# Optimization experiments

Measured on AMD Instinct MI355X. Metric: run time of the kernel, lower is better.

The kernel has to match this reference:

```python
import jax, jax.numpy as jnp
import numpy as np

B, S, D = 2, 2048, 512
H = 8
HD = D // H  # head dim = 64


def setup_inputs() -> dict:
    key = jax.random.key(0)
    ks = jax.random.split(key, 4)
    scale = 1.0 / np.sqrt(D)
    x = jax.random.normal(ks[0], (B, S, D), dtype=jnp.float32)
    wq = jax.random.normal(ks[1], (D, D), dtype=jnp.float32) * scale
    wk = jax.random.normal(ks[2], (D, D), dtype=jnp.float32) * scale
    wv = jax.random.normal(ks[3], (D, D), dtype=jnp.float32) * scale
    bq = jnp.zeros((D,), dtype=jnp.float32)
    bk = jnp.zeros((D,), dtype=jnp.float32)
    bv = jnp.zeros((D,), dtype=jnp.float32)
    return {"x": x, "wq": wq, "bq": bq, "wk": wk, "bk": bk, "wv": wv, "bv": bv}


def reference(x, wq, bq, wk, bk, wv, bv):
    # Linear projections (torch Linear: y = x @ W^T + b; weights here stored as [out,in])
    q = x @ wq.T + bq  # [B,S,D]
    k = x @ wk.T + bk
    v = x @ wv.T + bv
    # split heads -> [B,H,S,HD]
    q = q.reshape(B, S, H, HD).transpose(0, 2, 1, 3)
    k = k.reshape(B, S, H, HD).transpose(0, 2, 1, 3)
    v = v.reshape(B, S, H, HD).transpose(0, 2, 1, 3)
    # QK^T scores, scaled by 1/sqrt(head_dim)
    scores = jnp.einsum("bhqd,bhkd->bhqk", q, k) / jnp.sqrt(jnp.float32(HD))
    # softmax-free: elementwise sigmoid instead of softmax normalization
    attn = jax.nn.sigmoid(scores)  # [B,H,S,S] — the memory-bound intermediate
    out = jnp.einsum("bhqk,bhkd->bhqd", attn, v)
    # merge heads -> [B,S,D]
    return out.transpose(0, 2, 1, 3).reshape(B, S, D)
```

## Files before the change

kernel.cpp:

```cpp
#include <hip/hip_runtime.h>
#include <cstdint>
#include <cstddef>

#define BB   2
#define SS   2048
#define DD   512
#define HH   8
#define HDIM 64

typedef __attribute__((ext_vector_type(8)))  short          s16x8;
typedef __attribute__((ext_vector_type(8)))  unsigned short u16x8;
typedef __attribute__((ext_vector_type(16))) float          f32x16;

static __device__ __forceinline__ unsigned short f2bf(float f) {
  union { float f; unsigned u; } x; x.f = f;
  unsigned r = x.u + 0x7fffu + ((x.u >> 16) & 1u);
  return (unsigned short)(r >> 16);
}
static __device__ __forceinline__ unsigned packtrunc(float lo, float hi) {
  return __builtin_amdgcn_perm(__float_as_uint(hi), __float_as_uint(lo), 0x07060302u);
}

#define QSCALE (-0.18033688011111543f)

__global__ __launch_bounds__(256) void proj_kernel(
    const float* __restrict__ x,
    const float* __restrict__ wq, const float* __restrict__ wk, const float* __restrict__ wv,
    const float* __restrict__ bq, const float* __restrict__ bk, const float* __restrict__ bv,
    unsigned short* __restrict__ qo, unsigned short* __restrict__ ko,
    unsigned short* __restrict__ vt) {
  __shared__ unsigned short As[2][128 * 40];
  __shared__ unsigned short Bs[2][64 * 40];

  const int z = blockIdx.z;
  const float* w; const float* bias;
  if (z == 0)      { w = wq; bias = bq; }
  else if (z == 1) { w = wk; bias = bk; }
  else             { w = wv; bias = bv; }

  const int t = threadIdx.x;
  const int lane = t & 63, wave = t >> 6;
  const int ln = lane & 31, hi = lane >> 5;
  const int m0 = blockIdx.x * 128, n0 = blockIdx.y * 64;

  float4 ar[4], br[2];
#pragma unroll
  for (int i = 0; i < 4; i++) {
    int c = t + i * 256;
    ar[i] = *(const float4*)&x[(size_t)(m0 + (c >> 3)) * DD + (c & 7) * 4];
  }
#pragma unroll
  for (int i = 0; i < 2; i++) {
    int c = t + i * 256;
    br[i] = *(const float4*)&w[(size_t)(n0 + (c >> 3)) * DD + (c & 7) * 4];
  }
#pragma unroll
  for (int i = 0; i < 4; i++) {
    int c = t + i * 256;
    uint2 u; u.x = packtrunc(ar[i].x, ar[i].y); u.y = packtrunc(ar[i].z, ar[i].w);
    *(uint2*)&As[0][(c >> 3) * 40 + (c & 7) * 4] = u;
  }
#pragma unroll
  for (int i = 0; i < 2; i++) {
    int c = t + i * 256;
    uint2 u; u.x = packtrunc(br[i].x, br[i].y); u.y = packtrunc(br[i].z, br[i].w);
    *(uint2*)&Bs[0][(c >> 3) * 40 + (c & 7) * 4] = u;
  }
  __syncthreads();

  f32x16 acc0 = {}, acc1 = {};

#pragma unroll 2
  for (int kt = 0; kt < 16; kt++) {
    const int cur = kt & 1, nxt = cur ^ 1;
    if (kt < 15) {
      int k0 = (kt + 1) * 32;
#pragma unroll
      for (int i = 0; i < 4; i++) {
        int c = t + i * 256;
        ar[i] = *(const float4*)&x[(size_t)(m0 + (c >> 3)) * DD + k0 + (c & 7) * 4];
      }
#pragma unroll
      for (int i = 0; i < 2; i++) {
        int c = t + i * 256;
        br[i] = *(const float4*)&w[(size_t)(n0 + (c >> 3)) * DD + k0 + (c & 7) * 4];
      }
    }
#pragma unroll
    for (int c = 0; c < 2; c++) {
      s16x8 af = *(const s16x8*)&As[cur][(wave * 32 + ln) * 40 + c * 16 + hi * 8];
      s16x8 b0 = *(const s16x8*)&Bs[cur][(ln) * 40 + c * 16 + hi * 8];
      s16x8 b1 = *(const s16x8*)&Bs[cur][(32 + ln) * 40 + c * 16 + hi * 8];
      acc0 = __builtin_amdgcn_mfma_f32_32x32x16_bf16(af, b0, acc0, 0, 0, 0);
      acc1 = __builtin_amdgcn_mfma_f32_32x32x16_bf16(af, b1, acc1, 0, 0, 0);
    }
    if (kt < 15) {
#pragma unroll
      for (int i = 0; i < 4; i++) {
        int c = t + i * 256;
        uint2 u; u.x = packtrunc(ar[i].x, ar[i].y); u.y = packtrunc(ar[i].z, ar[i].w);
        *(uint2*)&As[nxt][(c >> 3) * 40 + (c & 7) * 4] = u;
      }
#pragma unroll
      for (int i = 0; i < 2; i++) {
        int c = t + i * 256;
        uint2 u; u.x = packtrunc(br[i].x, br[i].y); u.y = packtrunc(br[i].z, br[i].w);
        *(uint2*)&Bs[nxt][(c >> 3) * 40 + (c & 7) * 4] = u;
      }
    }
    __syncthreads();
  }

  const float scale = (z == 0) ? QSCALE : 1.0f;
  const int h = blockIdx.y;
  const int bidx = m0 >> 11;
  const int sbase = (m0 & 2047) + wave * 32;
  unsigned short* dst = (z == 0) ? qo : ko;
#pragma unroll
  for (int nh = 0; nh < 2; nh++) {
    f32x16 a = nh ? acc1 : acc0;
    float bval = bias[n0 + nh * 32 + ln];
    int hd = nh * 32 + ln;
    if (z < 2) {
#pragma unroll
      for (int r = 0; r < 16; r++) {
        int s = sbase + (r & 3) + 8 * (r >> 2) + 4 * hi;
        dst[(((size_t)(bidx * HH + h) * SS) + s) * HDIM + hd] = f2bf((a[r] + bval) * scale);
      }
    } else {
      size_t rowbase = (((size_t)(bidx * HH + h) * HDIM) + hd) * SS;
#pragma unroll
      for (int g = 0; g < 4; g++) {
#pragma unroll
        for (int j = 0; j < 4; j += 2) {
          int s = sbase + 8 * g + 4 * hi + j;
          unsigned pk = (unsigned)f2bf(a[g * 4 + j] + bval) |
                        ((unsigned)f2bf(a[g * 4 + j + 1] + bval) << 16);
          *(unsigned*)&vt[rowbase + s] = pk;
        }
      }
    }
  }
}

__global__ __launch_bounds__(256, 2) void attn_kernel(
    const unsigned short* __restrict__ qb,
    const unsigned short* __restrict__ kb,
    const unsigned short* __restrict__ vtb,
    float* __restrict__ out) {
  __shared__ __align__(16) float red[4 * 4096];

  const int t = threadIdx.x;
  const int lane = t & 63, wave = t >> 6;
  const int ln = lane & 31, hi = lane >> 5;
  const int fid = blockIdx.y * 32 + blockIdx.x;
  const int bh = fid & 15, qx = fid >> 4;
  const int b = bh >> 3, h = bh & 7;
  const unsigned short* qp = qb + (size_t)bh * SS * HDIM;
  const unsigned short* kp = kb + (size_t)bh * SS * HDIM;
  const unsigned short* vp = vtb + (size_t)bh * HDIM * SS;
  const int q0 = qx * 64;

  s16x8 qf[2][4];
#pragma unroll
  for (int qs = 0; qs < 2; qs++)
#pragma unroll
    for (int c = 0; c < 4; c++)
      qf[qs][c] = *(const s16x8*)&qp[(size_t)(q0 + qs * 32 + ln) * HDIM + c * 16 + hi * 8];

  f32x16 o00 = {}, o01 = {}, o10 = {}, o11 = {};

  s16x8 kf[2][4], vf[2][4];
  int koff = (wave * 32 + ln) * HDIM + hi * 8;
  int voff = ln * SS + wave * 32 + hi * 8;
#pragma unroll
  for (int c = 0; c < 4; c++) kf[0][c] = *(const s16x8*)&kp[koff + c * 16];
#pragma unroll
  for (int c = 0; c < 2; c++) {
    vf[0][c]     = *(const s16x8*)&vp[voff + c * 16];
    vf[0][2 + c] = *(const s16x8*)&vp[voff + 32 * SS + c * 16];
  }
  koff += 4 * 32 * HDIM;
  voff += 128;

#pragma unroll 2
  for (int i = 0; i < 16; i++) {
    const int cur = i & 1, nxt = cur ^ 1;
    if (i < 15) {
#pragma unroll
      for (int c = 0; c < 4; c++) kf[nxt][c] = *(const s16x8*)&kp[koff + c * 16];
#pragma unroll
      for (int c = 0; c < 2; c++) {
        vf[nxt][c]     = *(const s16x8*)&vp[voff + c * 16];
        vf[nxt][2 + c] = *(const s16x8*)&vp[voff + 32 * SS + c * 16];
      }
      koff += 4 * 32 * HDIM;
      voff += 128;
    }

    f32x16 st0 = {}, st1 = {};
#pragma unroll
    for (int c = 0; c < 4; c++) {
      st0 = __builtin_amdgcn_mfma_f32_32x32x16_bf16(kf[cur][c], qf[0][c], st0, 0, 0, 0);
      st1 = __builtin_amdgcn_mfma_f32_32x32x16_bf16(kf[cur][c], qf[1][c], st1, 0, 0, 0);
    }

    unsigned pgx[2][4], pgy[2][4];
#pragma unroll
    for (int qs = 0; qs < 2; qs++) {
      f32x16 stq = qs ? st1 : st0;
#pragma unroll
      for (int g = 0; g < 4; g++) {
        float p0 = __builtin_amdgcn_rcpf(1.0f + __builtin_amdgcn_exp2f(stq[4 * g + 0]));
        float p1 = __builtin_amdgcn_rcpf(1.0f + __builtin_amdgcn_exp2f(stq[4 * g + 1]));
        float p2 = __builtin_amdgcn_rcpf(1.0f + __builtin_amdgcn_exp2f(stq[4 * g + 2]));
        float p3 = __builtin_amdgcn_rcpf(1.0f + __builtin_amdgcn_exp2f(stq[4 * g + 3]));
        pgx[qs][g] = packtrunc(p0, p1);
        pgy[qs][g] = packtrunc(p2, p3);
      }
    }

#pragma unroll
    for (int c = 0; c < 2; c++) {
      const int gk = 2 * c + hi, gs = 2 * c + (hi ^ 1);
#pragma unroll
      for (int qs = 0; qs < 2; qs++) {
        unsigned rx = __shfl_xor((int)pgx[qs][gs], 32, 64);
        unsigned ry = __shfl_xor((int)pgy[qs][gs], 32, 64);
        union { unsigned u[4]; s16x8 v; } pu;
        pu.u[0] = hi ? rx : pgx[qs][gk];
        pu.u[1] = hi ? ry : pgy[qs][gk];
        pu.u[2] = hi ? pgx[qs][gk] : rx;
        pu.u[3] = hi ? pgy[qs][gk] : ry;
        if (qs == 0) {
          o00 = __builtin_amdgcn_mfma_f32_32x32x16_bf16(pu.v, vf[cur][c], o00, 0, 0, 0);
          o01 = __builtin_amdgcn_mfma_f32_32x32x16_bf16(pu.v, vf[cur][2 + c], o01, 0, 0, 0);
        } else {
          o10 = __builtin_amdgcn_mfma_f32_32x32x16_bf16(pu.v, vf[cur][c], o10, 0, 0, 0);
          o11 = __builtin_amdgcn_mfma_f32_32x32x16_bf16(pu.v, vf[cur][2 + c], o11, 0, 0, 0);
        }
      }
    }
  }

#pragma unroll
  for (int qs = 0; qs < 2; qs++)
#pragma unroll
    for (int dh = 0; dh < 2; dh++) {
      f32x16 ov = qs ? (dh ? o11 : o10) : (dh ? o01 : o00);
#pragma unroll
      for (int r = 0; r < 16; r++) {
        int ql = qs * 32 + (r & 3) + 8 * (r >> 2) + 4 * hi;
        red[wave * 4096 + ql * 64 + dh * 32 + ln] = ov[r];
      }
    }
  __syncthreads();
  const float4* red4 = (const float4*)red;
#pragma unroll
  for (int j = 0; j < 4; j++) {
    int g = t + j * 256;
    float4 s0 = red4[g], s1 = red4[1024 + g], s2 = red4[2048 + g], s3 = red4[3072 + g];
    float4 s;
    s.x = s0.x + s1.x + s2.x + s3.x;
    s.y = s0.y + s1.y + s2.y + s3.y;
    s.z = s0.z + s1.z + s2.z + s3.z;
    s.w = s0.w + s1.w + s2.w + s3.w;
    int q = g >> 4, dbase = (g & 15) * 4;
    *(float4*)&out[((size_t)(b * SS + q0 + q)) * DD + h * HDIM + dbase] = s;
  }
}

extern "C" void kernel_launch(void* const* d_in, const int* in_sizes, int n_in,
                              void* d_out, int out_size, void* d_ws, size_t ws_size,
                              hipStream_t stream) {
  const float* x  = (const float*)d_in[0];
  const float* wq = (const float*)d_in[1];
  const float* bq = (const float*)d_in[2];
  const float* wk = (const float*)d_in[3];
  const float* bk = (const float*)d_in[4];
  const float* wv = (const float*)d_in[5];
  const float* bv = (const float*)d_in[6];
  float* out = (float*)d_out;

  constexpr size_t XN = (size_t)BB * SS * DD;

  unsigned short* qo = (unsigned short*)d_ws;
  unsigned short* ko = qo + XN;
  unsigned short* vt = ko + XN;

  proj_kernel<<<dim3(32, 8, 3), 256, 0, stream>>>(x, wq, wk, wv, bq, bk, bv, qo, ko, vt);
  attn_kernel<<<dim3(SS / 64, BB * HH), 256, 0, stream>>>(qo, ko, vt, out);
}
```

Measured before the change: 125.3 us.

## Pre-swizzle K/V into fragment-contiguous layout and shrink projection tiles

The projection kernel now writes K and V directly in the per-lane MFMA fragment order, so the attention kernel loads each K/V fragment as one contiguous 16-byte chunk per lane instead of strided rows. The projection tile drops from 128x64 to 64x64 with a 2x2 wave grid, doubling its grid size. In the attention kernel the cross-wave reduction buffer is halved by having two waves accumulate in place, and launch bounds are raised to allow 4 blocks per CU. The trade-off is a more complex scattered store pattern in the projection epilogue and an extra synchronisation in the reduction.

New measurement: 334.7 us. 167% more time.

```diff
diff --git a/kernel.cpp b/kernel.cpp
--- a/kernel.cpp
+++ b/kernel.cpp
@@ -29,7 +29,7 @@
     const float* __restrict__ bq, const float* __restrict__ bk, const float* __restrict__ bv,
     unsigned short* __restrict__ qo, unsigned short* __restrict__ ko,
     unsigned short* __restrict__ vt) {
-  __shared__ unsigned short As[2][128 * 40];
+  __shared__ unsigned short As[2][64 * 40];
   __shared__ unsigned short Bs[2][64 * 40];
 
   const int z = blockIdx.z;
@@ -41,34 +41,28 @@
   const int t = threadIdx.x;
   const int lane = t & 63, wave = t >> 6;
   const int ln = lane & 31, hi = lane >> 5;
-  const int m0 = blockIdx.x * 128, n0 = blockIdx.y * 64;
-
-  float4 ar[4], br[2];
-#pragma unroll
-  for (int i = 0; i < 4; i++) {
+  const int wr = wave >> 1, wc = wave & 1;
+  const int m0 = blockIdx.x * 64, n0 = blockIdx.y * 64;
+
+  float4 ar[2], br[2];
+#pragma unroll
+  for (int i = 0; i < 2; i++) {
     int c = t + i * 256;
     ar[i] = *(const float4*)&x[(size_t)(m0 + (c >> 3)) * DD + (c & 7) * 4];
+    br[i] = *(const float4*)&w[(size_t)(n0 + (c >> 3)) * DD + (c & 7) * 4];
   }
 #pragma unroll
   for (int i = 0; i < 2; i++) {
     int c = t + i * 256;
-    br[i] = *(const float4*)&w[(size_t)(n0 + (c >> 3)) * DD + (c & 7) * 4];
-  }
-#pragma unroll
-  for (int i = 0; i < 4; i++) {
-    int c = t + i * 256;
-    uint2 u; u.x = packtrunc(ar[i].x, ar[i].y); u.y = packtrunc(ar[i].z, ar[i].w);
-    *(uint2*)&As[0][(c >> 3) * 40 + (c & 7) * 4] = u;
-  }
-#pragma unroll
-  for (int i = 0; i < 2; i++) {
-    int c = t + i * 256;
-    uint2 u; u.x = packtrunc(br[i].x, br[i].y); u.y = packtrunc(br[i].z, br[i].w);
-    *(uint2*)&Bs[0][(c >> 3) * 40 + (c & 7) * 4] = u;
+    uint2 ua, ub;
+    ua.x = packtrunc(ar[i].x, ar[i].y); ua.y = packtrunc(ar[i].z, ar[i].w);
+    ub.x = packtrunc(br[i].x, br[i].y); ub.y = packtrunc(br[i].z, br[i].w);
+    *(uint2*)&As[0][(c >> 3) * 40 + (c & 7) * 4] = ua;
+    *(uint2*)&Bs[0][(c >> 3) * 40 + (c & 7) * 4] = ub;
   }
   __syncthreads();
 
-  f32x16 acc0 = {}, acc1 = {};
+  f32x16 acc = {};
 
 #pragma unroll 2
   for (int kt = 0; kt < 16; kt++) {
@@ -76,79 +70,76 @@
     if (kt < 15) {
       int k0 = (kt + 1) * 32;
 #pragma unroll
-      for (int i = 0; i < 4; i++) {
+      for (int i = 0; i < 2; i++) {
         int c = t + i * 256;
         ar[i] = *(const float4*)&x[(size_t)(m0 + (c >> 3)) * DD + k0 + (c & 7) * 4];
-      }
+        br[i] = *(const float4*)&w[(size_t)(n0 + (c >> 3)) * DD + k0 + (c & 7) * 4];
+      }
+    }
+#pragma unroll
+    for (int c = 0; c < 2; c++) {
+      s16x8 af = *(const s16x8*)&As[cur][(wr * 32 + ln) * 40 + c * 16 + hi * 8];
+      s16x8 bf = *(const s16x8*)&Bs[cur][(wc * 32 + ln) * 40 + c * 16 + hi * 8];
+      acc = __builtin_amdgcn_mfma_f32_32x32x16_bf16(af, bf, acc, 0, 0, 0);
+    }
+    if (kt < 15) {
 #pragma unroll
       for (int i = 0; i < 2; i++) {
         int c = t + i * 256;
-        br[i] = *(const float4*)&w[(size_t)(n0 + (c >> 3)) * DD + k0 + (c & 7) * 4];
-      }
-    }
-#pragma unroll
-    for (int c = 0; c < 2; c++) {
-      s16x8 af = *(const s16x8*)&As[cur][(wave * 32 + ln) * 40 + c * 16 + hi * 8];
-      s16x8 b0 = *(const s16x8*)&Bs[cur][(ln) * 40 + c * 16 + hi * 8];
-      s16x8 b1 = *(const s16x8*)&Bs[cur][(32 + ln) * 40 + c * 16 + hi * 8];
-      acc0 = __builtin_amdgcn_mfma_f32_32x32x16_bf16(af, b0, acc0, 0, 0, 0);
-      acc1 = __builtin_amdgcn_mfma_f32_32x32x16_bf16(af, b1, acc1, 0, 0, 0);
-    }
-    if (kt < 15) {
-#pragma unroll
-      for (int i = 0; i < 4; i++) {
-        int c = t + i * 256;
-        uint2 u; u.x = packtrunc(ar[i].x, ar[i].y); u.y = packtrunc(ar[i].z, ar[i].w);
-        *(uint2*)&As[nxt][(c >> 3) * 40 + (c & 7) * 4] = u;
-      }
-#pragma unroll
-      for (int i = 0; i < 2; i++) {
-        int c = t + i * 256;
-        uint2 u; u.x = packtrunc(br[i].x, br[i].y); u.y = packtrunc(br[i].z, br[i].w);
-        *(uint2*)&Bs[nxt][(c >> 3) * 40 + (c & 7) * 4] = u;
+        uint2 ua, ub;
+        ua.x = packtrunc(ar[i].x, ar[i].y); ua.y = packtrunc(ar[i].z, ar[i].w);
+        ub.x = packtrunc(br[i].x, br[i].y); ub.y = packtrunc(br[i].z, br[i].w);
+        *(uint2*)&As[nxt][(c >> 3) * 40 + (c & 7) * 4] = ua;
+        *(uint2*)&Bs[nxt][(c >> 3) * 40 + (c & 7) * 4] = ub;
       }
     }
     __syncthreads();
   }
 
-  const float scale = (z == 0) ? QSCALE : 1.0f;
   const int h = blockIdx.y;
   const int bidx = m0 >> 11;
-  const int sbase = (m0 & 2047) + wave * 32;
-  unsigned short* dst = (z == 0) ? qo : ko;
-#pragma unroll
-  for (int nh = 0; nh < 2; nh++) {
-    f32x16 a = nh ? acc1 : acc0;
-    float bval = bias[n0 + nh * 32 + ln];
-    int hd = nh * 32 + ln;
-    if (z < 2) {
-#pragma unroll
-      for (int r = 0; r < 16; r++) {
-        int s = sbase + (r & 3) + 8 * (r >> 2) + 4 * hi;
-        dst[(((size_t)(bidx * HH + h) * SS) + s) * HDIM + hd] = f2bf((a[r] + bval) * scale);
-      }
-    } else {
-      size_t rowbase = (((size_t)(bidx * HH + h) * HDIM) + hd) * SS;
-#pragma unroll
-      for (int g = 0; g < 4; g++) {
-#pragma unroll
-        for (int j = 0; j < 4; j += 2) {
-          int s = sbase + 8 * g + 4 * hi + j;
-          unsigned pk = (unsigned)f2bf(a[g * 4 + j] + bval) |
-                        ((unsigned)f2bf(a[g * 4 + j + 1] + bval) << 16);
-          *(unsigned*)&vt[rowbase + s] = pk;
-        }
-      }
-    }
-  }
-}
-
-__global__ __launch_bounds__(256, 2) void attn_kernel(
+  const int sbase = (m0 & 2047) + wr * 32;
+  const int hd = wc * 32 + ln;
+  const float bval = bias[n0 + hd];
+  const size_t bhb = (size_t)(bidx * HH + h) * SS * HDIM;
+
+  if (z == 0) {
+#pragma unroll
+    for (int r = 0; r < 16; r++) {
+      int s = sbase + (r & 3) + 8 * (r >> 2) + 4 * hi;
+      qo[bhb + (size_t)s * HDIM + hd] = f2bf((acc[r] + bval) * QSCALE);
+    }
+  } else if (z == 1) {
+    const int c = hd >> 4, hk = (hd >> 3) & 1, j = hd & 7;
+    const int kts = sbase >> 5;
+    unsigned short* kd = ko + bhb + ((size_t)kts * 4 + c) * 512 + j;
+#pragma unroll
+    for (int r = 0; r < 16; r++) {
+      int off = (r & 3) + 8 * (r >> 2) + 4 * hi;
+      kd[(hk * 32 + off) * 8] = f2bf(acc[r] + bval);
+    }
+  } else {
+    const int kts = sbase >> 5;
+    unsigned short* vd = vt + bhb + ((size_t)kts * 4 + wc * 2) * 512 + ln * 8 + 4 * hi;
+#pragma unroll
+    for (int g = 0; g < 4; g++) {
+      unsigned short* vg = vd + ((g >> 1) * 512) + (g & 1) * 256;
+#pragma unroll
+      for (int j = 0; j < 4; j += 2) {
+        unsigned pk = (unsigned)f2bf(acc[g * 4 + j] + bval) |
+                      ((unsigned)f2bf(acc[g * 4 + j + 1] + bval) << 16);
+        *(unsigned*)&vg[j] = pk;
+      }
+    }
+  }
+}
+
+__global__ __launch_bounds__(256, 4) void attn_kernel(
     const unsigned short* __restrict__ qb,
-    const unsigned short* __restrict__ kb,
-    const unsigned short* __restrict__ vtb,
+    const unsigned short* __restrict__ kfb,
+    const unsigned short* __restrict__ vfb,
     float* __restrict__ out) {
-  __shared__ __align__(16) float red[4 * 4096];
+  __shared__ __align__(16) float red[2 * 4096];
 
   const int t = threadIdx.x;
   const int lane = t & 63, wave = t >> 6;
@@ -157,8 +148,8 @@
   const int bh = fid & 15, qx = fid >> 4;
   const int b = bh >> 3, h = bh & 7;
   const unsigned short* qp = qb + (size_t)bh * SS * HDIM;
-  const unsigned short* kp = kb + (size_t)bh * SS * HDIM;
-  const unsigned short* vp = vtb + (size_t)bh * HDIM * SS;
+  const unsigned short* kfp = kfb + (size_t)bh * SS * HDIM;
+  const unsigned short* vfp = vfb + (size_t)bh * SS * HDIM;
   const int q0 = qx * 64;
 
   s16x8 qf[2][4];
@@ -171,31 +162,25 @@
   f32x16 o00 = {}, o01 = {}, o10 = {}, o11 = {};
 
   s16x8 kf[2][4], vf[2][4];
-  int koff = (wave * 32 + ln) * HDIM + hi * 8;
-  int voff = ln * SS + wave * 32 + hi * 8;
-#pragma unroll
-  for (int c = 0; c < 4; c++) kf[0][c] = *(const s16x8*)&kp[koff + c * 16];
-#pragma unroll
-  for (int c = 0; c < 2; c++) {
-    vf[0][c]     = *(const s16x8*)&vp[voff + c * 16];
-    vf[0][2 + c] = *(const s16x8*)&vp[voff + 32 * SS + c * 16];
-  }
-  koff += 4 * 32 * HDIM;
-  voff += 128;
+  int koff = wave * 4 * 512 + lane * 8;
+  int voff = koff;
+#pragma unroll
+  for (int c = 0; c < 4; c++) {
+    kf[0][c] = *(const s16x8*)&kfp[koff + c * 512];
+    vf[0][c] = *(const s16x8*)&vfp[voff + c * 512];
+  }
+  koff += 8192; voff += 8192;
 
 #pragma unroll 2
   for (int i = 0; i < 16; i++) {
     const int cur = i & 1, nxt = cur ^ 1;
     if (i < 15) {
 #pragma unroll
-      for (int c = 0; c < 4; c++) kf[nxt][c] = *(const s16x8*)&kp[koff + c * 16];
-#pragma unroll
-      for (int c = 0; c < 2; c++) {
-        vf[nxt][c]     = *(const s16x8*)&vp[voff + c * 16];
-        vf[nxt][2 + c] = *(const s16x8*)&vp[voff + 32 * SS + c * 16];
-      }
-      koff += 4 * 32 * HDIM;
-      voff += 128;
+      for (int c = 0; c < 4; c++) {
+        kf[nxt][c] = *(const s16x8*)&kfp[koff + c * 512];
+        vf[nxt][c] = *(const s16x8*)&vfp[voff + c * 512];
+      }
+      koff += 8192; voff += 8192;
     }
 
     f32x16 st0 = {}, st1 = {};
@@ -243,28 +228,43 @@
     }
   }
 
-#pragma unroll
-  for (int qs = 0; qs < 2; qs++)
-#pragma unroll
-    for (int dh = 0; dh < 2; dh++) {
-      f32x16 ov = qs ? (dh ? o11 : o10) : (dh ? o01 : o00);
-#pragma unroll
-      for (int r = 0; r < 16; r++) {
-        int ql = qs * 32 + (r & 3) + 8 * (r >> 2) + 4 * hi;
-        red[wave * 4096 + ql * 64 + dh * 32 + ln] = ov[r];
-      }
-    }
+  if (wave >= 2) {
+#pragma unroll
+    for (int qs = 0; qs < 2; qs++)
+#pragma unroll
+      for (int dh = 0; dh < 2; dh++) {
+        f32x16 ov = qs ? (dh ? o11 : o10) : (dh ? o01 : o00);
+#pragma unroll
+        for (int r = 0; r < 16; r++) {
+          int ql = qs * 32 + (r & 3) + 8 * (r >> 2) + 4 * hi;
+          red[(wave - 2) * 4096 + ql * 64 + dh * 32 + ln] = ov[r];
+        }
+      }
+  }
   __syncthreads();
-  const float4* red4 = (const float4*)red;
+  if (wave < 2) {
+#pragma unroll
+    for (int qs = 0; qs < 2; qs++)
+#pragma unroll
+      for (int dh = 0; dh < 2; dh++) {
+        f32x16 ov = qs ? (dh ? o11 : o10) : (dh ? o01 : o00);
+#pragma unroll
+        for (int r = 0; r < 16; r++) {
+          int ql = qs * 32 + (r & 3) + 8 * (r >> 2) + 4 * hi;
+          int idx = wave * 4096 + ql * 64 + dh * 32 + ln;
+          red[idx] += ov[r];
+        }
+      }
+  }
+  __syncthreads();
+  const float4* r0 = (const float4*)red;
+  const float4* r1 = (const float4*)(red + 4096);
 #pragma unroll
   for (int j = 0; j < 4; j++) {
     int g = t + j * 256;
-    float4 s0 = red4[g], s1 = red4[1024 + g], s2 = red4[2048 + g], s3 = red4[3072 + g];
+    float4 s0 = r0[g], s1 = r1[g];
     float4 s;
-    s.x = s0.x + s1.x + s2.x + s3.x;
-    s.y = s0.y + s1.y + s2.y + s3.y;
-    s.z = s0.z + s1.z + s2.z + s3.z;
-    s.w = s0.w + s1.w + s2.w + s3.w;
+    s.x = s0.x + s1.x; s.y = s0.y + s1.y; s.z = s0.z + s1.z; s.w = s0.w + s1.w;
     int q = g >> 4, dbase = (g & 15) * 4;
     *(float4*)&out[((size_t)(b * SS + q0 + q)) * DD + h * HDIM + dbase] = s;
   }
@@ -288,6 +288,6 @@
   unsigned short* ko = qo + XN;
   unsigned short* vt = ko + XN;
 
-  proj_kernel<<<dim3(32, 8, 3), 256, 0, stream>>>(x, wq, wk, wv, bq, bk, bv, qo, ko, vt);
+  proj_kernel<<<dim3(64, 8, 3), 256, 0, stream>>>(x, wq, wk, wv, bq, bk, bv, qo, ko, vt);
   attn_kernel<<<dim3(SS / 64, BB * HH), 256, 0, stream>>>(qo, ko, vt, out);
 }
```
